# Kernel tuning notes

Hardware: AMD Instinct MI355X
Metric: run time of the kernel (lower is better)

## Reference

```python
import jax, jax.numpy as jnp
import numpy as np

B, T, L, H = 16384, 512, 4, 2  # batch, unroll_for, num_lstm, hidden_size (=input_size, hardcoded 2)


def setup_inputs() -> dict:
    key = jax.random.key(0)
    k0, k1, k2, k3, k4 = jax.random.split(key, 5)
    inputs = jax.random.normal(k0, (1, B, H), dtype=jnp.float32)
    labels = jax.random.normal(k1, (1, B, T, H), dtype=jnp.float32)
    # torch.nn.LSTMCell params, stacked over layers; gate order i, f, g, o.
    s = 1.0 / np.sqrt(H)
    W_ih = jax.random.uniform(k2, (L, 4 * H, H), dtype=jnp.float32, minval=-s, maxval=s)
    W_hh = jax.random.uniform(k3, (L, 4 * H, H), dtype=jnp.float32, minval=-s, maxval=s)
    b_hh = jax.random.uniform(k4, (L, 4 * H), dtype=jnp.float32, minval=-s, maxval=s)
    # bias_ih is force-zeroed and frozen in the original module -> omitted (identically zero).
    return {"inputs": inputs, "labels": labels, "W_ih": W_ih, "W_hh": W_hh, "b_hh": b_hh}


def _cell(x, h, c, wih, whh, bhh):
    # torch LSTMCell: gates = x W_ih^T + h W_hh^T + b_hh (b_ih == 0)
    g = x @ wih.T + h @ whh.T + bhh  # [B, 4H]
    i, f, gg, o = jnp.split(g, 4, axis=-1)
    c2 = jax.nn.sigmoid(f) * c + jax.nn.sigmoid(i) * jnp.tanh(gg)
    h2 = jax.nn.sigmoid(o) * jnp.tanh(c2)
    return h2, c2


def reference(inputs, labels, W_ih, W_hh, b_hh):
    x0 = inputs[0]          # [B, H]
    lab = labels[0]         # [B, T, H]
    n_layers = W_ih.shape[0]
    zeros = jnp.zeros((n_layers,) + x0.shape, dtype=x0.dtype)

    def step(carry, _):
        out, hs, cs = carry
        new_hs, new_cs = [], []
        for i in range(n_layers):  # small fixed layer count
            h, c = _cell(out, hs[i], cs[i], W_ih[i], W_hh[i], b_hh[i])
            new_hs.append(h)
            new_cs.append(c)
            out = h
        return (out, jnp.stack(new_hs), jnp.stack(new_cs)), out

    (_, _, _), outs = jax.lax.scan(step, (x0, zeros, zeros), None, length=lab.shape[1])
    ret = jnp.transpose(outs, (1, 0, 2))  # [B, T, H]
    loss = jnp.mean((ret - lab) ** 2)
    return ret, loss
```

## Files before the change

kernel.cpp:

```cpp
#include <hip/hip_runtime.h>

#define NB 16384
#define NT 512
#define NL 4
#define NH 2
#define NRET (NB*NT*NH)
#define TC 8

__device__ __forceinline__ float swap1(float x) {
  return __int_as_float(__builtin_amdgcn_mov_dpp(__float_as_int(x), 0xB1, 0xF, 0xF, true));
}
__device__ __forceinline__ float rcp1p(float e) {
  return __builtin_amdgcn_rcpf(1.0f + e);
}

__global__ __launch_bounds__(64, 1) void lstm_k(
    const float* __restrict__ inp, const float* __restrict__ lab,
    const float* __restrict__ Wih, const float* __restrict__ Whh,
    const float* __restrict__ bhh, float* __restrict__ out)
{
  __shared__ __align__(16) float lds[32][TC*NH];
  const int tid = threadIdx.x;
  const int el = tid >> 1, j = tid & 1, jo = j ^ 1;
  const int b0 = blockIdx.x << 5;
  const int b  = b0 + el;

  const float K1 = 1.4426950408889634f;
  const float K2 = 2.8853900817779268f;
  const float K4 = 5.7707801635558536f;

  float wio[NL][4], wix[NL][4], who[NL][4], whx[NL][4], bi[NL][4], part[NL][4];
  #pragma unroll
  for (int l = 0; l < NL; ++l) {
    #pragma unroll
    for (int g = 0; g < 4; ++g) {
      const int row = l*8 + g*2 + j;
      const float s = (g == 2) ? -K2 : -K1;
      wio[l][g] = s * Wih[row*2 + j];
      wix[l][g] = s * Wih[row*2 + jo];
      who[l][g] = s * Whh[row*2 + j];
      whx[l][g] = s * Whh[row*2 + jo];
      bi[l][g]  = s * bhh[row];
      part[l][g] = bi[l][g];
    }
  }

  float c[NL];
  #pragma unroll
  for (int l = 0; l < NL; ++l) c[l] = 0.f;

  float xo = inp[b*NH + j];
  float xx = inp[b*NH + jo];
  float lsum = 0.f;

  for (int t0 = 0; t0 < NT; t0 += TC) {
    float4 lv[2];
    #pragma unroll
    for (int q = 0; q < 2; ++q) {
      const int f = q*64 + tid, e = f >> 2, p = f & 3;
      lv[q] = ((const float4*)(lab + (size_t)(b0 + e) * (NT*NH) + (size_t)t0*NH))[p];
    }

    #pragma unroll
    for (int tl = 0; tl < TC; ++tl) {
      #pragma unroll
      for (int l = 0; l < NL; ++l) {
        float g0 = fmaf(wix[l][0], xx, fmaf(wio[l][0], xo, part[l][0]));
        float g1 = fmaf(wix[l][1], xx, fmaf(wio[l][1], xo, part[l][1]));
        float g2 = fmaf(wix[l][2], xx, fmaf(wio[l][2], xo, part[l][2]));
        float g3 = fmaf(wix[l][3], xx, fmaf(wio[l][3], xo, part[l][3]));
        float pi = rcp1p(__builtin_amdgcn_exp2f(g0));
        float pf = rcp1p(__builtin_amdgcn_exp2f(g1));
        float r2 = rcp1p(__builtin_amdgcn_exp2f(g2));
        float po = rcp1p(__builtin_amdgcn_exp2f(g3));
        float tgs = fmaf(-K4, r2, K2);
        c[l] = fmaf(pf, c[l], pi * tgs);
        float rc = rcp1p(__builtin_amdgcn_exp2f(c[l]));
        float po2 = po + po;
        float nh = fmaf(po2, rc, -po);
        float ns = swap1(nh);
        part[l][0] = fmaf(whx[l][0], ns, fmaf(who[l][0], nh, bi[l][0]));
        part[l][1] = fmaf(whx[l][1], ns, fmaf(who[l][1], nh, bi[l][1]));
        part[l][2] = fmaf(whx[l][2], ns, fmaf(who[l][2], nh, bi[l][2]));
        part[l][3] = fmaf(whx[l][3], ns, fmaf(who[l][3], nh, bi[l][3]));
        xo = nh; xx = ns;
      }
      lds[el][tl*NH + j] = xo;
    }
    __syncthreads();
    const float4* lf = (const float4*)&lds[0][0];
    #pragma unroll
    for (int q = 0; q < 2; ++q) {
      const int f = q*64 + tid, e = f >> 2, p = f & 3;
      float4 v = lf[f];
      float4* o4 = (float4*)(out + (size_t)(b0 + e) * (NT*NH) + (size_t)t0*NH);
      o4[p] = v;
      float d0 = v.x - lv[q].x, d1 = v.y - lv[q].y,
            d2 = v.z - lv[q].z, d3 = v.w - lv[q].w;
      lsum = fmaf(d0,d0, fmaf(d1,d1, fmaf(d2,d2, fmaf(d3,d3, lsum))));
    }
    __syncthreads();
  }

  #pragma unroll
  for (int off = 32; off >= 1; off >>= 1)
    lsum += __shfl_xor(lsum, off, 64);
  if (tid == 0)
    atomicAdd(out + NRET, lsum * (1.0f / (float)NRET));
}

extern "C" void kernel_launch(void* const* d_in, const int* in_sizes, int n_in,
                              void* d_out, int out_size, void* d_ws, size_t ws_size,
                              hipStream_t stream) {
  const float* inp = (const float*)d_in[0];
  const float* lab = (const float*)d_in[1];
  const float* Wih = (const float*)d_in[2];
  const float* Whh = (const float*)d_in[3];
  const float* bhh = (const float*)d_in[4];
  float* out = (float*)d_out;
  hipMemsetAsync(out + NRET, 0, sizeof(float), stream);
  lstm_k<<<NB/32, 64, 0, stream>>>(inp, lab, Wih, Whh, bhh, out);
}
```

Baseline: 198.3 us.

## Process two batch elements per lane pair to interleave independent LSTM chains

Each wave now handles 64 batch elements instead of 32, running two independent recurrence chains (A and B) interleaved to raise instruction-level parallelism and hide exp/rcp/DPP latency. Grid size is halved, LDS staging and label/output tiles doubled, and weights are pinned in VGPRs via empty asm. The trade-off is fewer waves across the device (one per CU), which may leave SIMDs idle, plus doubled register pressure.

Result: slower. 359.6 us (+81.3%).

```diff
diff --git a/kernel.cpp b/kernel.cpp
--- a/kernel.cpp
+++ b/kernel.cpp
@@ -19,17 +19,17 @@
     const float* __restrict__ Wih, const float* __restrict__ Whh,
     const float* __restrict__ bhh, float* __restrict__ out)
 {
-  __shared__ __align__(16) float lds[32][TC*NH];
+  __shared__ __align__(16) float lds[64][TC*NH];
   const int tid = threadIdx.x;
   const int el = tid >> 1, j = tid & 1, jo = j ^ 1;
-  const int b0 = blockIdx.x << 5;
-  const int b  = b0 + el;
+  const int b0 = blockIdx.x << 6;
+  const int bA = b0 + el, bB = b0 + 32 + el;
 
   const float K1 = 1.4426950408889634f;
   const float K2 = 2.8853900817779268f;
   const float K4 = 5.7707801635558536f;
 
-  float wio[NL][4], wix[NL][4], who[NL][4], whx[NL][4], bi[NL][4], part[NL][4];
+  float wio[NL][4], wix[NL][4], who[NL][4], whx[NL][4], bi[NL][4];
   #pragma unroll
   for (int l = 0; l < NL; ++l) {
     #pragma unroll
@@ -41,22 +41,33 @@
       who[l][g] = s * Whh[row*2 + j];
       whx[l][g] = s * Whh[row*2 + jo];
       bi[l][g]  = s * bhh[row];
-      part[l][g] = bi[l][g];
     }
   }
+  #pragma unroll
+  for (int l = 0; l < NL; ++l)
+    asm volatile("" :
+      "+v"(wio[l][0]), "+v"(wio[l][1]), "+v"(wio[l][2]), "+v"(wio[l][3]),
+      "+v"(wix[l][0]), "+v"(wix[l][1]), "+v"(wix[l][2]), "+v"(wix[l][3]),
+      "+v"(who[l][0]), "+v"(who[l][1]), "+v"(who[l][2]), "+v"(who[l][3]),
+      "+v"(whx[l][0]), "+v"(whx[l][1]), "+v"(whx[l][2]), "+v"(whx[l][3]),
+      "+v"(bi[l][0]),  "+v"(bi[l][1]),  "+v"(bi[l][2]),  "+v"(bi[l][3]));
 
-  float c[NL];
+  float partA[NL][4], partB[NL][4], cA[NL], cB[NL];
   #pragma unroll
-  for (int l = 0; l < NL; ++l) c[l] = 0.f;
+  for (int l = 0; l < NL; ++l) {
+    cA[l] = 0.f; cB[l] = 0.f;
+    #pragma unroll
+    for (int g = 0; g < 4; ++g) { partA[l][g] = bi[l][g]; partB[l][g] = bi[l][g]; }
+  }
 
-  float xo = inp[b*NH + j];
-  float xx = inp[b*NH + jo];
+  float xoA = inp[bA*NH + j], xxA = inp[bA*NH + jo];
+  float xoB = inp[bB*NH + j], xxB = inp[bB*NH + jo];
   float lsum = 0.f;
 
   for (int t0 = 0; t0 < NT; t0 += TC) {
-    float4 lv[2];
+    float4 lv[4];
     #pragma unroll
-    for (int q = 0; q < 2; ++q) {
+    for (int q = 0; q < 4; ++q) {
       const int f = q*64 + tid, e = f >> 2, p = f & 3;
       lv[q] = ((const float4*)(lab + (size_t)(b0 + e) * (NT*NH) + (size_t)t0*NH))[p];
     }
@@ -65,32 +76,52 @@
     for (int tl = 0; tl < TC; ++tl) {
       #pragma unroll
       for (int l = 0; l < NL; ++l) {
-        float g0 = fmaf(wix[l][0], xx, fmaf(wio[l][0], xo, part[l][0]));
-        float g1 = fmaf(wix[l][1], xx, fmaf(wio[l][1], xo, part[l][1]));
-        float g2 = fmaf(wix[l][2], xx, fmaf(wio[l][2], xo, part[l][2]));
-        float g3 = fmaf(wix[l][3], xx, fmaf(wio[l][3], xo, part[l][3]));
-        float pi = rcp1p(__builtin_amdgcn_exp2f(g0));
-        float pf = rcp1p(__builtin_amdgcn_exp2f(g1));
-        float r2 = rcp1p(__builtin_amdgcn_exp2f(g2));
-        float po = rcp1p(__builtin_amdgcn_exp2f(g3));
-        float tgs = fmaf(-K4, r2, K2);
-        c[l] = fmaf(pf, c[l], pi * tgs);
-        float rc = rcp1p(__builtin_amdgcn_exp2f(c[l]));
-        float po2 = po + po;
-        float nh = fmaf(po2, rc, -po);
-        float ns = swap1(nh);
-        part[l][0] = fmaf(whx[l][0], ns, fmaf(who[l][0], nh, bi[l][0]));
-        part[l][1] = fmaf(whx[l][1], ns, fmaf(who[l][1], nh, bi[l][1]));
-        part[l][2] = fmaf(whx[l][2], ns, fmaf(who[l][2], nh, bi[l][2]));
-        part[l][3] = fmaf(whx[l][3], ns, fmaf(who[l][3], nh, bi[l][3]));
-        xo = nh; xx = ns;
+        float a0 = fmaf(wix[l][0], xxA, fmaf(wio[l][0], xoA, partA[l][0]));
+        float a1 = fmaf(wix[l][1], xxA, fmaf(wio[l][1], xoA, partA[l][1]));
+        float a2 = fmaf(wix[l][2], xxA, fmaf(wio[l][2], xoA, partA[l][2]));
+        float a3 = fmaf(wix[l][3], xxA, fmaf(wio[l][3], xoA, partA[l][3]));
+        float b0g = fmaf(wix[l][0], xxB, fmaf(wio[l][0], xoB, partB[l][0]));
+        float b1g = fmaf(wix[l][1], xxB, fmaf(wio[l][1], xoB, partB[l][1]));
+        float b2g = fmaf(wix[l][2], xxB, fmaf(wio[l][2], xoB, partB[l][2]));
+        float b3g = fmaf(wix[l][3], xxB, fmaf(wio[l][3], xoB, partB[l][3]));
+
+        float piA = rcp1p(__builtin_amdgcn_exp2f(a0));
+        float pfA = rcp1p(__builtin_amdgcn_exp2f(a1));
+        float r2A = rcp1p(__builtin_amdgcn_exp2f(a2));
+        float poA = rcp1p(__builtin_amdgcn_exp2f(a3));
+        float piB = rcp1p(__builtin_amdgcn_exp2f(b0g));
+        float pfB = rcp1p(__builtin_amdgcn_exp2f(b1g));
+        float r2B = rcp1p(__builtin_amdgcn_exp2f(b2g));
+        float poB = rcp1p(__builtin_amdgcn_exp2f(b3g));
+
+        float tgA = fmaf(-K4, r2A, K2);
+        float tgB = fmaf(-K4, r2B, K2);
+        cA[l] = fmaf(pfA, cA[l], piA * tgA);
+        cB[l] = fmaf(pfB, cB[l], piB * tgB);
+        float rcA = rcp1p(__builtin_amdgcn_exp2f(cA[l]));
+        float rcB = rcp1p(__builtin_amdgcn_exp2f(cB[l]));
+        float nhA = fmaf(poA + poA, rcA, -poA);
+        float nhB = fmaf(poB + poB, rcB, -poB);
+        float nsA = swap1(nhA);
+        float nsB = swap1(nhB);
+        partA[l][0] = fmaf(whx[l][0], nsA, fmaf(who[l][0], nhA, bi[l][0]));
+        partA[l][1] = fmaf(whx[l][1], nsA, fmaf(who[l][1], nhA, bi[l][1]));
+        partA[l][2] = fmaf(whx[l][2], nsA, fmaf(who[l][2], nhA, bi[l][2]));
+        partA[l][3] = fmaf(whx[l][3], nsA, fmaf(who[l][3], nhA, bi[l][3]));
+        partB[l][0] = fmaf(whx[l][0], nsB, fmaf(who[l][0], nhB, bi[l][0]));
+        partB[l][1] = fmaf(whx[l][1], nsB, fmaf(who[l][1], nhB, bi[l][1]));
+        partB[l][2] = fmaf(whx[l][2], nsB, fmaf(who[l][2], nhB, bi[l][2]));
+        partB[l][3] = fmaf(whx[l][3], nsB, fmaf(who[l][3], nhB, bi[l][3]));
+        xoA = nhA; xxA = nsA;
+        xoB = nhB; xxB = nsB;
       }
-      lds[el][tl*NH + j] = xo;
+      lds[el][tl*NH + j]      = xoA;
+      lds[32 + el][tl*NH + j] = xoB;
     }
     __syncthreads();
     const float4* lf = (const float4*)&lds[0][0];
     #pragma unroll
-    for (int q = 0; q < 2; ++q) {
+    for (int q = 0; q < 4; ++q) {
       const int f = q*64 + tid, e = f >> 2, p = f & 3;
       float4 v = lf[f];
       float4* o4 = (float4*)(out + (size_t)(b0 + e) * (NT*NH) + (size_t)t0*NH);
@@ -119,5 +150,5 @@
   const float* bhh = (const float*)d_in[4];
   float* out = (float*)d_out;
   hipMemsetAsync(out + NRET, 0, sizeof(float), stream);
-  lstm_k<<<NB/32, 64, 0, stream>>>(inp, lab, Wih, Whh, bhh, out);
+  lstm_k<<<NB/64, 64, 0, stream>>>(inp, lab, Wih, Whh, bhh, out);
 }
```
